# Performance work log

Measured on AMD Instinct MI355X. Metric: run time of the kernel, lower is better.

## Reference

```python
import jax, jax.numpy as jnp
import numpy as np

H = 256
EDGE_DIM = 16
B, N = 8, 4096
E = 524288
EPS = 1e-5


def setup_inputs() -> dict:
    key = jax.random.key(0)
    ks = jax.random.split(key, 16)
    s = 0.02
    return {
        "h": jax.random.normal(ks[0], (B, N, H), dtype=jnp.float32),
        "edge_index": jax.random.randint(ks[1], (2, E), 0, B * N, dtype=jnp.int64),
        "edge_attr": jax.random.normal(ks[2], (E, EDGE_DIM), dtype=jnp.float32),
        "mask": jnp.ones((B, N), dtype=jnp.float32),
        # message_net params
        "W1": jax.random.normal(ks[3], (2 * H + EDGE_DIM, H), dtype=jnp.float32) * s,
        "b1": jnp.zeros((H,), dtype=jnp.float32),
        "W2": jax.random.normal(ks[4], (H, H), dtype=jnp.float32) * s,
        "b2": jnp.zeros((H,), dtype=jnp.float32),
        # update_net params
        "U1": jax.random.normal(ks[5], (2 * H, H), dtype=jnp.float32) * s,
        "c1": jnp.zeros((H,), dtype=jnp.float32),
        "U2": jax.random.normal(ks[6], (H, H), dtype=jnp.float32) * s,
        "c2": jnp.zeros((H,), dtype=jnp.float32),
        # LayerNorm params
        "gamma": jnp.ones((H,), dtype=jnp.float32),
        "beta": jnp.zeros((H,), dtype=jnp.float32),
    }


def reference(h, edge_index, edge_attr, mask, W1, b1, W2, b2, U1, c1, U2, c2, gamma, beta):
    batch, n_nodes, hid = h.shape
    h_flat = h.reshape(-1, hid)                       # (B*N, H)
    src, dst = edge_index[0], edge_index[1]
    # gather -> message MLP
    msg_in = jnp.concatenate([h_flat[src], h_flat[dst], edge_attr], axis=-1)  # (E, 2H+16)
    messages = jax.nn.silu(msg_in @ W1 + b1) @ W2 + b2                        # (E, H)
    # scatter-add aggregation by destination node
    aggr = jax.ops.segment_sum(messages, dst, num_segments=batch * n_nodes)   # (B*N, H)
    # update MLP + residual (dropout = identity in eval mode)
    upd_in = jnp.concatenate([h_flat, aggr], axis=-1)                         # (B*N, 2H)
    h_new = h_flat + (jax.nn.silu(upd_in @ U1 + c1) @ U2 + c2)
    # LayerNorm over last dim
    mu = jnp.mean(h_new, axis=-1, keepdims=True)
    var = jnp.mean(jnp.square(h_new - mu), axis=-1, keepdims=True)
    h_new = (h_new - mu) * jax.lax.rsqrt(var + EPS) * gamma + beta
    return h_new.reshape(batch, n_nodes, hid) * mask[..., None]
```

## Files before the change

### kernel.cpp

```cpp
#include <hip/hip_runtime.h>

#define H_DIM 256
#define E_NUM 524288
#define NN    32768
#define K2    512
#define K2S   520
#define SAS   264
#define XS    264
#define NPW   4

typedef unsigned short u16;
typedef unsigned int   u32;
typedef __attribute__((ext_vector_type(8))) short s16x8;
typedef __attribute__((ext_vector_type(4))) float f32x4;
typedef __attribute__((ext_vector_type(2))) float f32x2;
typedef __attribute__((ext_vector_type(4))) unsigned short u16x4;

__device__ __forceinline__ u16 f2b(float x) {
    u32 u = __float_as_uint(x);
    u32 r = (u + 0x7FFFu + ((u >> 16) & 1u)) >> 16;
    return (u16)r;
}
__device__ __forceinline__ float b2f(u16 v) {
    u32 u = ((u32)v) << 16;
    return __uint_as_float(u);
}
__device__ __forceinline__ float fsig(float x) {
    return __builtin_amdgcn_rcpf(1.f + __expf(-x));
}

__global__ __launch_bounds__(256) void k_prep_w(
    const float* __restrict__ W1, const float* __restrict__ W2,
    const float* __restrict__ U1, const float* __restrict__ U2,
    u16* __restrict__ WpqT, u16* __restrict__ W2T,
    u16* __restrict__ U1T, u16* __restrict__ U2T) {
    int idx = blockIdx.x * 256 + threadIdx.x;
    if (idx < 131072) {
        int c = idx >> 8, k = idx & 255;
        float v = (c < 256) ? W1[k * 256 + c] : W1[(256 + k) * 256 + (c - 256)];
        WpqT[idx] = f2b(v);
    } else if (idx < 196608) {
        int i = idx - 131072; int c = i >> 8, k = i & 255;
        W2T[i] = f2b(W2[k * 256 + c]);
    } else if (idx < 327680) {
        int i = idx - 196608; int c = i >> 9, k = i & 511;
        U1T[i] = f2b(U1[(size_t)k * 256 + c]);
    } else if (idx < 393216) {
        int i = idx - 327680; int c = i >> 8, k = i & 255;
        U2T[i] = f2b(U2[k * 256 + c]);
    }
}

__global__ __launch_bounds__(256) void k_hist(const int* __restrict__ eidx,
                                              int* __restrict__ cnt) {
    int i = blockIdx.x * 256 + threadIdx.x;
    if (i < E_NUM) atomicAdd(&cnt[eidx[E_NUM + i]], 1);
}

__global__ __launch_bounds__(256) void k_scan(const int* __restrict__ cnt,
                                              int* __restrict__ base,
                                              int* __restrict__ nxt) {
    __shared__ int part[256];
    const int t = threadIdx.x;
    const int st = t * 128;
    int s = 0;
    for (int i = 0; i < 128; ++i) s += cnt[st + i];
    part[t] = s;
    __syncthreads();
    if (t == 0) {
        int r = 0;
        for (int i = 0; i < 256; ++i) { int v = part[i]; part[i] = r; r += v; }
        base[NN] = r;
    }
    __syncthreads();
    int off = part[t];
    for (int i = 0; i < 128; ++i) {
        int v = cnt[st + i];
        base[st + i] = off;
        nxt[st + i] = off;
        off += v;
    }
}

__global__ __launch_bounds__(256) void k_scatter(const int* __restrict__ eidx,
                                                 int* __restrict__ nxt,
                                                 int2* __restrict__ elist) {
    int i = blockIdx.x * 256 + threadIdx.x;
    if (i < E_NUM) {
        int d = eidx[E_NUM + i];
        int p = atomicAdd(&nxt[d], 1);
        elist[p] = make_int2(eidx[i], i);
    }
}

__global__ __launch_bounds__(256, 2) void k_gemm_pq(
    const float* __restrict__ h, const u16* __restrict__ WpqT,
    u16* __restrict__ PQ) {
    __shared__ __align__(16) u16 sA[64 * SAS];
    const int t = threadIdx.x;
    const int rowTile = blockIdx.x >> 1, q = blockIdx.x & 1;
    const int n0 = rowTile * 64;
    {
        const int r = t >> 2, g = t & 3;
        const float* hrow = h + (size_t)(n0 + r) * 256;
        u16* rowp = sA + r * SAS;
#pragma unroll
        for (int j = 0; j < 8; ++j) {
            const int c = g + 4 * j;
            float4 v0 = *reinterpret_cast<const float4*>(hrow + c * 8);
            float4 v1 = *reinterpret_cast<const float4*>(hrow + c * 8 + 4);
            s16x8 o;
            o[0] = (short)f2b(v0.x); o[1] = (short)f2b(v0.y);
            o[2] = (short)f2b(v0.z); o[3] = (short)f2b(v0.w);
            o[4] = (short)f2b(v1.x); o[5] = (short)f2b(v1.y);
            o[6] = (short)f2b(v1.z); o[7] = (short)f2b(v1.w);
            *reinterpret_cast<s16x8*>(rowp + c * 8) = o;
        }
    }
    __syncthreads();
    const int lane = t & 63, wv = t >> 6;
    const int l15 = lane & 15, l4 = lane >> 4;
    const int colBase = wv * 64 + l15;
    const f32x4 z4 = {0.f, 0.f, 0.f, 0.f};
    f32x4 acc[4][4];
#pragma unroll
    for (int m = 0; m < 4; ++m)
#pragma unroll
        for (int n = 0; n < 4; ++n) acc[m][n] = z4;
    {
        const u16* Bb = WpqT + (size_t)(q * 256 + colBase) * 256 + l4 * 8;
        for (int kk = 0; kk < 8; ++kk) {
            s16x8 a[4], b[4];
#pragma unroll
            for (int m = 0; m < 4; ++m)
                a[m] = *reinterpret_cast<const s16x8*>(sA + (m * 16 + l15) * SAS + kk * 32 + l4 * 8);
#pragma unroll
            for (int n = 0; n < 4; ++n)
                b[n] = *reinterpret_cast<const s16x8*>(Bb + (size_t)n * 16 * 256 + kk * 32);
#pragma unroll
            for (int m = 0; m < 4; ++m)
#pragma unroll
                for (int n = 0; n < 4; ++n)
                    acc[m][n] = __builtin_amdgcn_mfma_f32_16x16x32_bf16(a[m], b[n], acc[m][n], 0, 0, 0);
        }
    }
#pragma unroll
    for (int m = 0; m < 4; ++m)
#pragma unroll
        for (int j = 0; j < 4; ++j) {
            const int row = n0 + m * 16 + l4 * 4 + j;
            u16* op = PQ + (size_t)row * 512 + q * 256 + colBase;
#pragma unroll
            for (int n = 0; n < 4; ++n) op[n * 16] = f2b(acc[m][n][j]);
        }
}

__global__ __launch_bounds__(256, 4) void k_aggr(
    const u16* __restrict__ PQ, const int2* __restrict__ elist,
    const int* __restrict__ base, const float* __restrict__ ea,
    const float* __restrict__ W1, const float* __restrict__ b1,
    u16* __restrict__ Sb) {
    const int t = threadIdx.x, lane = t & 63, wv = t >> 6;
    const int c0 = lane * 4;
    f32x2 WrL[16], WrH[16];
#pragma unroll
    for (int k = 0; k < 16; ++k) {
        float4 w = *reinterpret_cast<const float4*>(W1 + (size_t)(512 + k) * 256 + c0);
        WrL[k] = f32x2{w.x, w.y};
        WrH[k] = f32x2{w.z, w.w};
    }
    const float4 b1v = *reinterpret_cast<const float4*>(b1 + c0);

    const int dBase = (blockIdx.x * 4 + wv) * NPW;
    for (int nn = 0; nn < NPW; ++nn) {
        const int d = dBase + nn;
        f32x2 qbL = {b1v.x, b1v.y}, qbH = {b1v.z, b1v.w};
        {
            u16x4 qv = *reinterpret_cast<const u16x4*>(PQ + (size_t)d * 512 + 256 + c0);
            qbL[0] += b2f(qv.x); qbL[1] += b2f(qv.y);
            qbH[0] += b2f(qv.z); qbH[1] += b2f(qv.w);
        }
        const int e0 = base[d], e1 = base[d + 1];
        f32x2 accL = {0.f, 0.f}, accH = {0.f, 0.f};
        for (int cb = e0; cb < e1; cb += 64) {
            const int n = min(64, e1 - cb);
            int2 ee = make_int2(0, 0);
            if (lane < n) ee = elist[cb + lane];
            int src = __shfl(ee.x, 0), eid = __shfl(ee.y, 0);
            u16x4 pv = *reinterpret_cast<const u16x4*>(PQ + (size_t)src * 512 + c0);
            const float* ep = ea + (size_t)eid * 16;
            float4 a0 = *reinterpret_cast<const float4*>(ep);
            float4 a1 = *reinterpret_cast<const float4*>(ep + 4);
            float4 a2 = *reinterpret_cast<const float4*>(ep + 8);
            float4 a3 = *reinterpret_cast<const float4*>(ep + 12);
            for (int k = 0; k < n; ++k) {
                const u16x4 pc = pv;
                const float4 e0v = a0, e1v = a1, e2v = a2, e3v = a3;
                if (k + 1 < n) {
                    src = __shfl(ee.x, k + 1); eid = __shfl(ee.y, k + 1);
                    pv = *reinterpret_cast<const u16x4*>(PQ + (size_t)src * 512 + c0);
                    const float* ep2 = ea + (size_t)eid * 16;
                    a0 = *reinterpret_cast<const float4*>(ep2);
                    a1 = *reinterpret_cast<const float4*>(ep2 + 4);
                    a2 = *reinterpret_cast<const float4*>(ep2 + 8);
                    a3 = *reinterpret_cast<const float4*>(ep2 + 12);
                }
                f32x2 xL = qbL, xH = qbH;
                xL[0] += b2f(pc.x); xL[1] += b2f(pc.y);
                xH[0] += b2f(pc.z); xH[1] += b2f(pc.w);
                xL = xL + WrL[0]  * e0v.x; xH = xH + WrH[0]  * e0v.x;
                xL = xL + WrL[1]  * e0v.y; xH = xH + WrH[1]  * e0v.y;
                xL = xL + WrL[2]  * e0v.z; xH = xH + WrH[2]  * e0v.z;
                xL = xL + WrL[3]  * e0v.w; xH = xH + WrH[3]  * e0v.w;
                xL = xL + WrL[4]  * e1v.x; xH = xH + WrH[4]  * e1v.x;
                xL = xL + WrL[5]  * e1v.y; xH = xH + WrH[5]  * e1v.y;
                xL = xL + WrL[6]  * e1v.z; xH = xH + WrH[6]  * e1v.z;
                xL = xL + WrL[7]  * e1v.w; xH = xH + WrH[7]  * e1v.w;
                xL = xL + WrL[8]  * e2v.x; xH = xH + WrH[8]  * e2v.x;
                xL = xL + WrL[9]  * e2v.y; xH = xH + WrH[9]  * e2v.y;
                xL = xL + WrL[10] * e2v.z; xH = xH + WrH[10] * e2v.z;
                xL = xL + WrL[11] * e2v.w; xH = xH + WrH[11] * e2v.w;
                xL = xL + WrL[12] * e3v.x; xH = xH + WrH[12] * e3v.x;
                xL = xL + WrL[13] * e3v.y; xH = xH + WrH[13] * e3v.y;
                xL = xL + WrL[14] * e3v.z; xH = xH + WrH[14] * e3v.z;
                xL = xL + WrL[15] * e3v.w; xH = xH + WrH[15] * e3v.w;
                accL[0] += xL[0] * fsig(xL[0]);
                accL[1] += xL[1] * fsig(xL[1]);
                accH[0] += xH[0] * fsig(xH[0]);
                accH[1] += xH[1] * fsig(xH[1]);
            }
        }
        u16x4 o;
        o.x = f2b(accL[0]); o.y = f2b(accL[1]);
        o.z = f2b(accH[0]); o.w = f2b(accH[1]);
        *reinterpret_cast<u16x4*>(Sb + (size_t)d * 256 + c0) = o;
    }
}

__global__ __launch_bounds__(256, 2) void k_post(
    const float* __restrict__ h, const u16* __restrict__ Sb,
    const u16* __restrict__ W2T, const int* __restrict__ base,
    const float* __restrict__ b2,
    const u16* __restrict__ U1T, const u16* __restrict__ U2T,
    const float* __restrict__ c1, const float* __restrict__ c2,
    const float* __restrict__ gamma, const float* __restrict__ beta,
    const float* __restrict__ mask,
    float* __restrict__ out) {
    __shared__ __align__(16) char smemraw[64 * XS * 4];
    u16* sA = reinterpret_cast<u16*>(smemraw);
    const int t  = threadIdx.x;
    const int n0 = blockIdx.x * 64;

    {
        const int r = t >> 2, g = t & 3;
        const int node = n0 + r;
        const float* hrow = h + (size_t)node * H_DIM;
        const u16* srow = Sb + (size_t)node * H_DIM;
        u16* rowp = sA + r * K2S;
#pragma unroll
        for (int j = 0; j < 16; ++j) {
            const int c = g + 4 * j;
            if (c < 32) {
                float4 v0 = *reinterpret_cast<const float4*>(hrow + c * 8);
                float4 v1 = *reinterpret_cast<const float4*>(hrow + c * 8 + 4);
                s16x8 o;
                o[0] = (short)f2b(v0.x); o[1] = (short)f2b(v0.y);
                o[2] = (short)f2b(v0.z); o[3] = (short)f2b(v0.w);
                o[4] = (short)f2b(v1.x); o[5] = (short)f2b(v1.y);
                o[6] = (short)f2b(v1.z); o[7] = (short)f2b(v1.w);
                *reinterpret_cast<s16x8*>(rowp + c * 8) = o;
            } else {
                const int cc = c - 32;
                *reinterpret_cast<s16x8*>(rowp + 256 + cc * 8) =
                    *reinterpret_cast<const s16x8*>(srow + cc * 8);
            }
        }
    }
    __syncthreads();

    const int lane = t & 63, wv = t >> 6;
    const int l15 = lane & 15, l4 = lane >> 4;
    const int colBase = wv * 64 + l15;
    const f32x4 z4 = {0.f, 0.f, 0.f, 0.f};

    f32x4 acc[4][4];
#pragma unroll
    for (int m = 0; m < 4; ++m)
#pragma unroll
        for (int n = 0; n < 4; ++n) acc[m][n] = z4;

    {
        const u16* Bb = W2T + (size_t)colBase * 256 + l4 * 8;
        for (int kk = 0; kk < 8; ++kk) {
            s16x8 a[4], b[4];
#pragma unroll
            for (int m = 0; m < 4; ++m)
                a[m] = *reinterpret_cast<const s16x8*>(sA + (m * 16 + l15) * K2S + 256 + kk * 32 + l4 * 8);
#pragma unroll
            for (int n = 0; n < 4; ++n)
                b[n] = *reinterpret_cast<const s16x8*>(Bb + (size_t)n * 16 * 256 + kk * 32);
#pragma unroll
            for (int m = 0; m < 4; ++m)
#pragma unroll
                for (int n = 0; n < 4; ++n)
                    acc[m][n] = __builtin_amdgcn_mfma_f32_16x16x32_bf16(a[m], b[n], acc[m][n], 0, 0, 0);
        }
    }
    __syncthreads();

    {
        float b2v[4];
#pragma unroll
        for (int n = 0; n < 4; ++n) b2v[n] = b2[colBase + n * 16];
#pragma unroll
        for (int m = 0; m < 4; ++m)
#pragma unroll
            for (int j = 0; j < 4; ++j) {
                const int row = m * 16 + l4 * 4 + j;
                const float dv = (float)(base[n0 + row + 1] - base[n0 + row]);
#pragma unroll
                for (int n = 0; n < 4; ++n)
                    sA[row * K2S + 256 + colBase + n * 16] = f2b(acc[m][n][j] + dv * b2v[n]);
            }
    }
    __syncthreads();

#pragma unroll
    for (int m = 0; m < 4; ++m)
#pragma unroll
        for (int n = 0; n < 4; ++n) acc[m][n] = z4;
    {
        const u16* Bb = U1T + (size_t)colBase * K2 + l4 * 8;
        for (int kk = 0; kk < 16; ++kk) {
            s16x8 a[4], b[4];
#pragma unroll
            for (int m = 0; m < 4; ++m)
                a[m] = *reinterpret_cast<const s16x8*>(sA + (m * 16 + l15) * K2S + kk * 32 + l4 * 8);
#pragma unroll
            for (int n = 0; n < 4; ++n)
                b[n] = *reinterpret_cast<const s16x8*>(Bb + (size_t)n * 16 * K2 + kk * 32);
#pragma unroll
            for (int m = 0; m < 4; ++m)
#pragma unroll
                for (int n = 0; n < 4; ++n)
                    acc[m][n] = __builtin_amdgcn_mfma_f32_16x16x32_bf16(a[m], b[n], acc[m][n], 0, 0, 0);
        }
    }
    __syncthreads();

    {
        u16* sX = reinterpret_cast<u16*>(smemraw);
        float c1v[4];
#pragma unroll
        for (int n = 0; n < 4; ++n) c1v[n] = c1[colBase + n * 16];
#pragma unroll
        for (int m = 0; m < 4; ++m)
#pragma unroll
            for (int n = 0; n < 4; ++n)
#pragma unroll
                for (int j = 0; j < 4; ++j) {
                    float x = acc[m][n][j] + c1v[n];
                    float s = x * fsig(x);
                    sX[(m * 16 + l4 * 4 + j) * XS + colBase + n * 16] = f2b(s);
                }
    }
    __syncthreads();

#pragma unroll
    for (int m = 0; m < 4; ++m)
#pragma unroll
        for (int n = 0; n < 4; ++n) acc[m][n] = z4;
    {
        const u16* sX = reinterpret_cast<u16*>(smemraw);
        const u16* Bb = U2T + (size_t)colBase * H_DIM + l4 * 8;
        for (int kk = 0; kk < 8; ++kk) {
            s16x8 a[4], b[4];
#pragma unroll
            for (int m = 0; m < 4; ++m)
                a[m] = *reinterpret_cast<const s16x8*>(sX + (m * 16 + l15) * XS + kk * 32 + l4 * 8);
#pragma unroll
            for (int n = 0; n < 4; ++n)
                b[n] = *reinterpret_cast<const s16x8*>(Bb + (size_t)n * 16 * H_DIM + kk * 32);
#pragma unroll
            for (int m = 0; m < 4; ++m)
#pragma unroll
                for (int n = 0; n < 4; ++n)
                    acc[m][n] = __builtin_amdgcn_mfma_f32_16x16x32_bf16(a[m], b[n], acc[m][n], 0, 0, 0);
        }
    }
    __syncthreads();

    {
        float* sF = reinterpret_cast<float*>(smemraw);
        float c2v[4];
#pragma unroll
        for (int n = 0; n < 4; ++n) c2v[n] = c2[colBase + n * 16];
#pragma unroll
        for (int m = 0; m < 4; ++m)
#pragma unroll
            for (int n = 0; n < 4; ++n)
#pragma unroll
                for (int j = 0; j < 4; ++j) {
                    const int row = m * 16 + l4 * 4 + j;
                    const float hv = h[(size_t)(n0 + row) * H_DIM + colBase + n * 16];
                    sF[row * XS + colBase + n * 16] = acc[m][n][j] + c2v[n] + hv;
                }
    }
    __syncthreads();

    {
        const float* sF = reinterpret_cast<const float*>(smemraw);
        const int rr = t >> 2, p = t & 3;
        const float* rowf = sF + rr * XS + p * 64;
        float s1 = 0.f, s2 = 0.f;
#pragma unroll
        for (int i = 0; i < 64; ++i) { float v = rowf[i]; s1 += v; s2 += v * v; }
        s1 += __shfl_xor(s1, 1); s1 += __shfl_xor(s1, 2);
        s2 += __shfl_xor(s2, 1); s2 += __shfl_xor(s2, 2);
        const float mu   = s1 * (1.f / 256.f);
        const float var  = s2 * (1.f / 256.f) - mu * mu;
        const float rstd = rsqrtf(var + 1e-5f);
        const int node = n0 + rr;
        const float mk = mask[node];
        float* op = out + (size_t)node * H_DIM + p * 64;
        const float* gp = gamma + p * 64;
        const float* bp = beta + p * 64;
#pragma unroll
        for (int i = 0; i < 64; i += 4) {
            float4 x  = *reinterpret_cast<const float4*>(rowf + i);
            float4 g4 = *reinterpret_cast<const float4*>(gp + i);
            float4 b4 = *reinterpret_cast<const float4*>(bp + i);
            float4 o;
            o.x = (((x.x - mu) * rstd) * g4.x + b4.x) * mk;
            o.y = (((x.y - mu) * rstd) * g4.y + b4.y) * mk;
            o.z = (((x.z - mu) * rstd) * g4.z + b4.z) * mk;
            o.w = (((x.w - mu) * rstd) * g4.w + b4.w) * mk;
            *reinterpret_cast<float4*>(op + i) = o;
        }
    }
}

#define OFF_PQ     0ull
#define OFF_SB     33554432ull
#define OFF_WPQT   50331648ull
#define OFF_W2T    50593792ull
#define OFF_U1T    50724864ull
#define OFF_U2T    50987008ull
#define OFF_CNT    51118080ull
#define OFF_BASE   51249152ull
#define OFF_NEXT   51380480ull
#define OFF_ELIST  51511552ull

extern "C" void kernel_launch(void* const* d_in, const int* in_sizes, int n_in,
                              void* d_out, int out_size, void* d_ws, size_t ws_size,
                              hipStream_t stream) {
    const float* h     = (const float*)d_in[0];
    const int*   eidx  = (const int*)d_in[1];
    const float* ea    = (const float*)d_in[2];
    const float* mask  = (const float*)d_in[3];
    const float* W1    = (const float*)d_in[4];
    const float* b1    = (const float*)d_in[5];
    const float* W2    = (const float*)d_in[6];
    const float* b2    = (const float*)d_in[7];
    const float* U1    = (const float*)d_in[8];
    const float* c1    = (const float*)d_in[9];
    const float* U2    = (const float*)d_in[10];
    const float* c2    = (const float*)d_in[11];
    const float* gamma = (const float*)d_in[12];
    const float* beta  = (const float*)d_in[13];
    float* out = (float*)d_out;
    char*  ws  = (char*)d_ws;

    u16*  PQ    = (u16*)(ws + OFF_PQ);
    u16*  Sb    = (u16*)(ws + OFF_SB);
    u16*  WpqT  = (u16*)(ws + OFF_WPQT);
    u16*  W2T   = (u16*)(ws + OFF_W2T);
    u16*  U1T   = (u16*)(ws + OFF_U1T);
    u16*  U2T   = (u16*)(ws + OFF_U2T);
    int*  cnt   = (int*)(ws + OFF_CNT);
    int*  base  = (int*)(ws + OFF_BASE);
    int*  nxt   = (int*)(ws + OFF_NEXT);
    int2* elist = (int2*)(ws + OFF_ELIST);

    hipMemsetAsync(cnt, 0, (size_t)NN * sizeof(int), stream);

    k_prep_w<<<1536, 256, 0, stream>>>(W1, W2, U1, U2, WpqT, W2T, U1T, U2T);
    k_hist<<<E_NUM / 256, 256, 0, stream>>>(eidx, cnt);
    k_scan<<<1, 256, 0, stream>>>(cnt, base, nxt);
    k_scatter<<<E_NUM / 256, 256, 0, stream>>>(eidx, nxt, elist);
    k_gemm_pq<<<(NN / 64) * 2, 256, 0, stream>>>(h, WpqT, PQ);
    k_aggr<<<NN / (4 * NPW), 256, 0, stream>>>(PQ, elist, base, ea, W1, b1, Sb);
    k_post<<<NN / 64, 256, 0, stream>>>(h, Sb, W2T, base, b2, U1T, U2T,
                                        c1, c2, gamma, beta, mask, out);
}
```

Measured before the change: 326.5 us.

## Prefetch eight gathered rows ahead and shuffle edge attributes in edge aggregation

The per-destination edge loop now keeps eight outstanding gathers of the projected source rows in flight instead of one. Each lane loads its own edge's 16 attributes once, and they are broadcast with lane shuffles rather than every lane loading all attributes for every edge. The scan kernel also replaces the serial single-thread prefix over 256 partials with a wave shuffle scan, and the count-summing loop is unrolled. The changes target gather latency and redundant global loads, at the cost of more registers (eight u16x4 buffers plus 16 shuffled floats) and many more shuffle instructions per edge.

After: 528.7 us. 1.62x slower.

```diff
diff --git a/kernel.cpp b/kernel.cpp
--- a/kernel.cpp
+++ b/kernel.cpp
@@ -60,20 +60,25 @@
 __global__ __launch_bounds__(256) void k_scan(const int* __restrict__ cnt,
                                               int* __restrict__ base,
                                               int* __restrict__ nxt) {
-    __shared__ int part[256];
-    const int t = threadIdx.x;
+    __shared__ int wsum[4];
+    const int t = threadIdx.x, lane = t & 63, w = t >> 6;
     const int st = t * 128;
     int s = 0;
+#pragma unroll 8
     for (int i = 0; i < 128; ++i) s += cnt[st + i];
-    part[t] = s;
-    __syncthreads();
-    if (t == 0) {
-        int r = 0;
-        for (int i = 0; i < 256; ++i) { int v = part[i]; part[i] = r; r += v; }
-        base[NN] = r;
-    }
-    __syncthreads();
-    int off = part[t];
+    int sc = s;
+#pragma unroll
+    for (int off = 1; off < 64; off <<= 1) {
+        int v = __shfl_up(sc, off);
+        if (lane >= off) sc += v;
+    }
+    if (lane == 63) wsum[w] = sc;
+    __syncthreads();
+    int woff = 0;
+    for (int i = 0; i < w; ++i) woff += wsum[i];
+    const int excl = woff + sc - s;
+    if (t == 255) base[NN] = woff + sc;
+    int off = excl;
     for (int i = 0; i < 128; ++i) {
         int v = cnt[st + i];
         base[st + i] = off;
@@ -180,55 +185,70 @@
             qbL[0] += b2f(qv.x); qbL[1] += b2f(qv.y);
             qbH[0] += b2f(qv.z); qbH[1] += b2f(qv.w);
         }
-        const int e0 = base[d], e1 = base[d + 1];
+        const int eBeg = base[d];
+        const int nAll = base[d + 1] - eBeg;
         f32x2 accL = {0.f, 0.f}, accH = {0.f, 0.f};
-        for (int cb = e0; cb < e1; cb += 64) {
-            const int n = min(64, e1 - cb);
-            int2 ee = make_int2(0, 0);
-            if (lane < n) ee = elist[cb + lane];
-            int src = __shfl(ee.x, 0), eid = __shfl(ee.y, 0);
-            u16x4 pv = *reinterpret_cast<const u16x4*>(PQ + (size_t)src * 512 + c0);
-            const float* ep = ea + (size_t)eid * 16;
-            float4 a0 = *reinterpret_cast<const float4*>(ep);
-            float4 a1 = *reinterpret_cast<const float4*>(ep + 4);
-            float4 a2 = *reinterpret_cast<const float4*>(ep + 8);
-            float4 a3 = *reinterpret_cast<const float4*>(ep + 12);
-            for (int k = 0; k < n; ++k) {
-                const u16x4 pc = pv;
-                const float4 e0v = a0, e1v = a1, e2v = a2, e3v = a3;
-                if (k + 1 < n) {
-                    src = __shfl(ee.x, k + 1); eid = __shfl(ee.y, k + 1);
-                    pv = *reinterpret_cast<const u16x4*>(PQ + (size_t)src * 512 + c0);
-                    const float* ep2 = ea + (size_t)eid * 16;
-                    a0 = *reinterpret_cast<const float4*>(ep2);
-                    a1 = *reinterpret_cast<const float4*>(ep2 + 4);
-                    a2 = *reinterpret_cast<const float4*>(ep2 + 8);
-                    a3 = *reinterpret_cast<const float4*>(ep2 + 12);
-                }
+
+        for (int cb = 0; cb < nAll; cb += 64) {
+            const int m = min(64, nAll - cb);
+            const int2 ee = elist[eBeg + cb + min(lane, m - 1)];
+            const float* myep = ea + (size_t)ee.y * 16;
+            const float4 w0 = *reinterpret_cast<const float4*>(myep);
+            const float4 w1 = *reinterpret_cast<const float4*>(myep + 4);
+            const float4 w2 = *reinterpret_cast<const float4*>(myep + 8);
+            const float4 w3 = *reinterpret_cast<const float4*>(myep + 12);
+
+            auto gather = [&](int idx) -> u16x4 {
+                const int s = __shfl(ee.x, idx);
+                return *reinterpret_cast<const u16x4*>(PQ + (size_t)s * 512 + c0);
+            };
+            auto edge_compute = [&](int k, const u16x4& pc) {
                 f32x2 xL = qbL, xH = qbH;
                 xL[0] += b2f(pc.x); xL[1] += b2f(pc.y);
                 xH[0] += b2f(pc.z); xH[1] += b2f(pc.w);
-                xL = xL + WrL[0]  * e0v.x; xH = xH + WrH[0]  * e0v.x;
-                xL = xL + WrL[1]  * e0v.y; xH = xH + WrH[1]  * e0v.y;
-                xL = xL + WrL[2]  * e0v.z; xH = xH + WrH[2]  * e0v.z;
-                xL = xL + WrL[3]  * e0v.w; xH = xH + WrH[3]  * e0v.w;
-                xL = xL + WrL[4]  * e1v.x; xH = xH + WrH[4]  * e1v.x;
-                xL = xL + WrL[5]  * e1v.y; xH = xH + WrH[5]  * e1v.y;
-                xL = xL + WrL[6]  * e1v.z; xH = xH + WrH[6]  * e1v.z;
-                xL = xL + WrL[7]  * e1v.w; xH = xH + WrH[7]  * e1v.w;
-                xL = xL + WrL[8]  * e2v.x; xH = xH + WrH[8]  * e2v.x;
-                xL = xL + WrL[9]  * e2v.y; xH = xH + WrH[9]  * e2v.y;
-                xL = xL + WrL[10] * e2v.z; xH = xH + WrH[10] * e2v.z;
-                xL = xL + WrL[11] * e2v.w; xH = xH + WrH[11] * e2v.w;
-                xL = xL + WrL[12] * e3v.x; xH = xH + WrH[12] * e3v.x;
-                xL = xL + WrL[13] * e3v.y; xH = xH + WrH[13] * e3v.y;
-                xL = xL + WrL[14] * e3v.z; xH = xH + WrH[14] * e3v.z;
-                xL = xL + WrL[15] * e3v.w; xH = xH + WrH[15] * e3v.w;
+                float e;
+                e = __shfl(w0.x, k); xL = xL + WrL[0]  * e; xH = xH + WrH[0]  * e;
+                e = __shfl(w0.y, k); xL = xL + WrL[1]  * e; xH = xH + WrH[1]  * e;
+                e = __shfl(w0.z, k); xL = xL + WrL[2]  * e; xH = xH + WrH[2]  * e;
+                e = __shfl(w0.w, k); xL = xL + WrL[3]  * e; xH = xH + WrH[3]  * e;
+                e = __shfl(w1.x, k); xL = xL + WrL[4]  * e; xH = xH + WrH[4]  * e;
+                e = __shfl(w1.y, k); xL = xL + WrL[5]  * e; xH = xH + WrH[5]  * e;
+                e = __shfl(w1.z, k); xL = xL + WrL[6]  * e; xH = xH + WrH[6]  * e;
+                e = __shfl(w1.w, k); xL = xL + WrL[7]  * e; xH = xH + WrH[7]  * e;
+                e = __shfl(w2.x, k); xL = xL + WrL[8]  * e; xH = xH + WrH[8]  * e;
+                e = __shfl(w2.y, k); xL = xL + WrL[9]  * e; xH = xH + WrH[9]  * e;
+                e = __shfl(w2.z, k); xL = xL + WrL[10] * e; xH = xH + WrH[10] * e;
+                e = __shfl(w2.w, k); xL = xL + WrL[11] * e; xH = xH + WrH[11] * e;
+                e = __shfl(w3.x, k); xL = xL + WrL[12] * e; xH = xH + WrH[12] * e;
+                e = __shfl(w3.y, k); xL = xL + WrL[13] * e; xH = xH + WrH[13] * e;
+                e = __shfl(w3.z, k); xL = xL + WrL[14] * e; xH = xH + WrH[14] * e;
+                e = __shfl(w3.w, k); xL = xL + WrL[15] * e; xH = xH + WrH[15] * e;
                 accL[0] += xL[0] * fsig(xL[0]);
                 accL[1] += xL[1] * fsig(xL[1]);
                 accH[0] += xH[0] * fsig(xH[0]);
                 accH[1] += xH[1] * fsig(xH[1]);
+            };
+
+            u16x4 p0 = gather(0), p1 = gather(1), p2 = gather(2), p3 = gather(3);
+            u16x4 p4 = gather(4), p5 = gather(5), p6 = gather(6), p7 = gather(7);
+            int kb = 0;
+            for (; kb + 8 <= m; kb += 8) {
+                edge_compute(kb + 0, p0); p0 = gather(min(kb + 8,  63));
+                edge_compute(kb + 1, p1); p1 = gather(min(kb + 9,  63));
+                edge_compute(kb + 2, p2); p2 = gather(min(kb + 10, 63));
+                edge_compute(kb + 3, p3); p3 = gather(min(kb + 11, 63));
+                edge_compute(kb + 4, p4); p4 = gather(min(kb + 12, 63));
+                edge_compute(kb + 5, p5); p5 = gather(min(kb + 13, 63));
+                edge_compute(kb + 6, p6); p6 = gather(min(kb + 14, 63));
+                edge_compute(kb + 7, p7); p7 = gather(min(kb + 15, 63));
             }
+            if (kb + 0 < m) edge_compute(kb + 0, p0);
+            if (kb + 1 < m) edge_compute(kb + 1, p1);
+            if (kb + 2 < m) edge_compute(kb + 2, p2);
+            if (kb + 3 < m) edge_compute(kb + 3, p3);
+            if (kb + 4 < m) edge_compute(kb + 4, p4);
+            if (kb + 5 < m) edge_compute(kb + 5, p5);
+            if (kb + 6 < m) edge_compute(kb + 6, p6);
         }
         u16x4 o;
         o.x = f2b(accL[0]); o.y = f2b(accL[1]);
```
